# Kernel tuning notes

Measured on AMD Instinct MI355X. Metric: run time of the kernel, lower is better.

The kernel has to match this reference:

```python
import jax, jax.numpy as jnp
import numpy as np

B, S, HID, NH, HD, E, K = 8, 1024, 1024, 16, 64, 8, 2
IDIM = 2 * HD  # expert internal dim
EPS = 1e-5


def layer_norm(x, g, b):
    m = jnp.mean(x, axis=-1, keepdims=True)
    v = jnp.mean(jnp.square(x - m), axis=-1, keepdims=True)
    return (x - m) * jax.lax.rsqrt(v + EPS) * g + b


def setup_inputs() -> dict:
    key = jax.random.key(0)
    ks = jax.random.split(key, 12)
    n = jax.random.normal
    return {
        "queries": n(ks[0], (B, S, HID), jnp.float32),
        "keys": n(ks[1], (B, S, HID), jnp.float32),
        "values": n(ks[2], (B, S, HID), jnp.float32),
        "memorys": n(ks[3], (B, NH, S, HD), jnp.float32),
        "Wq": n(ks[4], (HD, HD), jnp.float32) * 0.02,
        "Wk": n(ks[5], (HD, HD), jnp.float32) * 0.02,
        "Wv": n(ks[6], (HD, HD), jnp.float32) * 0.02,
        "forget_gate": n(ks[7], (HD,), jnp.float32),
        "gate_W": n(ks[8], (E, HD), jnp.float32) * 0.02,
        "gate_b": jnp.zeros((E,), jnp.float32),
        "ln1_g": jnp.ones((E, HD), jnp.float32),
        "ln1_b": jnp.zeros((E, HD), jnp.float32),
        "W1": n(ks[9], (E, IDIM, HD), jnp.float32) * 0.02,
        "ln2_g": jnp.ones((E, IDIM), jnp.float32),
        "ln2_b": jnp.zeros((E, IDIM), jnp.float32),
        "W2": n(ks[10], (E, HD, IDIM), jnp.float32) * 0.02,
        "b2": jnp.zeros((E, HD), jnp.float32),
    }


def reference(queries, keys, values, memorys, Wq, Wk, Wv, forget_gate,
              gate_W, gate_b, ln1_g, ln1_b, W1, ln2_g, ln2_b, W2, b2):
    bsz, seq, _ = queries.shape
    gelu = lambda x: jax.nn.gelu(x, approximate=False)

    # head split: [B,S,HID] -> [B,NH,S,HD]
    q = queries.reshape(bsz, seq, NH, HD).transpose(0, 2, 1, 3)
    k = keys.reshape(bsz, seq, NH, HD).transpose(0, 2, 1, 3)
    v = values.reshape(bsz, seq, NH, HD).transpose(0, 2, 1, 3)

    q_ = q @ Wq.T
    k_ = k @ Wk.T
    v_ = v @ Wv.T

    # gated memory cell
    cell = k_ * v_ + forget_gate * memorys
    current_memorys = (1.0 - forget_gate) * cell + forget_gate * memorys
    cell_values = q_ * current_memorys  # [B,NH,S,HD]

    # token-mixing MoE (per-token, over last dim)
    x = cell_values.reshape(-1, HD)  # [N, HD], N = B*NH*S
    logits = x @ gate_W.T + gate_b  # [N, E]
    topv, topi = jax.lax.top_k(logits, K)  # [N, K]
    # sparse combine weights [N, E] (raw gate values, as in the original)
    w = jnp.sum(jax.nn.one_hot(topi, E, dtype=x.dtype) * topv[..., None], axis=1)

    def expert_fwd(g1, b1, w1, g2, b2_, w2, bias2):
        h = gelu(layer_norm(x, g1, b1)) @ w1.T      # [N, IDIM]
        h = gelu(layer_norm(h, g2, b2_)) @ w2.T + bias2  # [N, HD]
        return h

    all_out = jax.vmap(expert_fwd)(ln1_g, ln1_b, W1, ln2_g, ln2_b, W2, b2)  # [E,N,HD]
    moe = jnp.einsum('ne,end->nd', w, all_out)  # [N, HD]

    token_mixing = moe.reshape(bsz, NH, seq, HD).transpose(0, 2, 1, 3).reshape(bsz, seq, NH * HD)
    return token_mixing, current_memorys
```

## Files before the change

### kernel.cpp

```cpp
#include <hip/hip_runtime.h>
#include <stdint.h>

typedef unsigned short u16;
typedef unsigned int   u32;
typedef unsigned long long u64;
typedef __attribute__((ext_vector_type(8))) short short8;
typedef __attribute__((ext_vector_type(4))) short s16x4;
typedef __attribute__((ext_vector_type(4))) float f32x4;

#define B_    8
#define S_    1024
#define HID_  1024
#define NH_   16
#define HD_   64
#define E_    8
#define IDIM_ 128
#define NTOK  (B_*NH_*S_)

#define CSTRIDE 16

__device__ __forceinline__ float bf2f(u16 u){ return __uint_as_float(((u32)u) << 16); }
__device__ __forceinline__ u16 f2bf(float f){
    u32 u = __float_as_uint(f);
    u32 r = u + 0x7fffu + ((u >> 16) & 1u);
    return (u16)(r >> 16);
}
__device__ __forceinline__ short8 frag8(const float* __restrict__ p){
    float4 a = *(const float4*)p;
    float4 b = *(const float4*)(p + 4);
    short8 r;
    r[0]=(short)f2bf(a.x); r[1]=(short)f2bf(a.y); r[2]=(short)f2bf(a.z); r[3]=(short)f2bf(a.w);
    r[4]=(short)f2bf(b.x); r[5]=(short)f2bf(b.y); r[6]=(short)f2bf(b.z); r[7]=(short)f2bf(b.w);
    return r;
}
__device__ __forceinline__ float gelu_exact(float x){
    return 0.5f * x * (1.0f + erff(x * 0.70710678118654752f));
}
__device__ __forceinline__ float gelu_f(float x){
    float z = 1.5957691216057308f * (x + 0.044715f * x * x * x);
    float e = __expf(z);
    float t = 1.0f - 2.0f / (e + 1.0f);
    return 0.5f * x * (1.0f + t);
}

__global__ void k_zero(u32* c){
    c[threadIdx.x] = 0;
}

__global__ __launch_bounds__(256) void k_prep(
    const float* __restrict__ W1, const float* __restrict__ W2,
    u16* __restrict__ wB1, u16* __restrict__ wB2, u32* __restrict__ counters)
{
    const int i = blockIdx.x*256 + threadIdx.x;
    if (blockIdx.x == 0) counters[threadIdx.x] = 0;
    wB1[i] = f2bf(W1[i]);
    wB2[i] = f2bf(W2[i]);
}

__global__ __launch_bounds__(256,4) void k_proj(
    const float* __restrict__ qin, const float* __restrict__ kin, const float* __restrict__ vin,
    const float* __restrict__ mem,
    const float* __restrict__ Wq, const float* __restrict__ Wk, const float* __restrict__ Wv,
    const float* __restrict__ fg,
    float* __restrict__ cur_out, float* __restrict__ out0)
{
    const int lane = threadIdx.x & 63;
    const int wid  = threadIdx.x >> 6;
    const int m    = lane & 15;
    const int kg   = lane >> 4;

    const int slab  = blockIdx.x;
    const int chunk = slab & 7, h = (slab >> 3) & 15, b = slab >> 7;
    const int tw    = chunk*128 + wid*32;

    const float* kbase = kin + ((size_t)b*S_)*HID_ + h*64;
    const float* vbase = vin + ((size_t)b*S_)*HID_ + h*64;
    const float* qbase = qin + ((size_t)b*S_)*HID_ + h*64;

    f32x4 accK[2][4], accV[2][4];
    const f32x4 z = {0.f,0.f,0.f,0.f};
    #pragma unroll
    for (int i=0;i<2;i++){ accK[i][0]=z;accK[i][1]=z;accK[i][2]=z;accK[i][3]=z;
                           accV[i][0]=z;accV[i][1]=z;accV[i][2]=z;accV[i][3]=z; }

    #pragma unroll
    for (int kk=0; kk<2; kk++){
        const int k0 = kk*32 + kg*8;
        short8 aF[2], bF[4];
        #pragma unroll
        for (int mt=0; mt<2; mt++) aF[mt] = frag8(kbase + (size_t)(tw + mt*16 + m)*HID_ + k0);
        #pragma unroll
        for (int ct=0; ct<4; ct++) bF[ct] = frag8(Wk + (ct*16 + m)*64 + k0);
        #pragma unroll
        for (int mt=0; mt<2; mt++)
            #pragma unroll
            for (int ct=0; ct<4; ct++)
                accK[mt][ct] = __builtin_amdgcn_mfma_f32_16x16x32_bf16(aF[mt], bF[ct], accK[mt][ct], 0,0,0);
    }
    #pragma unroll
    for (int kk=0; kk<2; kk++){
        const int k0 = kk*32 + kg*8;
        short8 aF[2], bF[4];
        #pragma unroll
        for (int mt=0; mt<2; mt++) aF[mt] = frag8(vbase + (size_t)(tw + mt*16 + m)*HID_ + k0);
        #pragma unroll
        for (int ct=0; ct<4; ct++) bF[ct] = frag8(Wv + (ct*16 + m)*64 + k0);
        #pragma unroll
        for (int mt=0; mt<2; mt++)
            #pragma unroll
            for (int ct=0; ct<4; ct++)
                accV[mt][ct] = __builtin_amdgcn_mfma_f32_16x16x32_bf16(aF[mt], bF[ct], accV[mt][ct], 0,0,0);
    }

    const size_t nb = ((size_t)(b*NH_ + h)) << 10;
    float fgv[4];
    #pragma unroll
    for (int ct=0; ct<4; ct++) fgv[ct] = fg[ct*16 + m];

    #pragma unroll
    for (int mt=0; mt<2; mt++){
        #pragma unroll
        for (int r=0; r<4; r++){
            const int tok = tw + mt*16 + kg*4 + r;
            const size_t rowo = (nb + (size_t)tok)*64;
            #pragma unroll
            for (int ct=0; ct<4; ct++){
                const int d = ct*16 + m;
                const float kd = accK[mt][ct][r];
                const float vd = accV[mt][ct][r];
                const float f  = fgv[ct];
                const float mv = mem[rowo + d];
                const float cell = kd*vd + f*mv;
                const float cur  = (1.0f - f)*cell + f*mv;
                accK[mt][ct][r] = cur;
                cur_out[rowo + d] = cur;
            }
        }
    }

    f32x4 accQ[2][4];
    #pragma unroll
    for (int i=0;i<2;i++){ accQ[i][0]=z;accQ[i][1]=z;accQ[i][2]=z;accQ[i][3]=z; }

    #pragma unroll
    for (int kk=0; kk<2; kk++){
        const int k0 = kk*32 + kg*8;
        short8 aF[2], bF[4];
        #pragma unroll
        for (int mt=0; mt<2; mt++) aF[mt] = frag8(qbase + (size_t)(tw + mt*16 + m)*HID_ + k0);
        #pragma unroll
        for (int ct=0; ct<4; ct++) bF[ct] = frag8(Wq + (ct*16 + m)*64 + k0);
        #pragma unroll
        for (int mt=0; mt<2; mt++)
            #pragma unroll
            for (int ct=0; ct<4; ct++)
                accQ[mt][ct] = __builtin_amdgcn_mfma_f32_16x16x32_bf16(aF[mt], bF[ct], accQ[mt][ct], 0,0,0);
    }

    #pragma unroll
    for (int mt=0; mt<2; mt++){
        #pragma unroll
        for (int r=0; r<4; r++){
            const int tok = tw + mt*16 + kg*4 + r;
            const size_t po = ((size_t)(b*S_ + tok)*NH_ + h)*64;
            #pragma unroll
            for (int ct=0; ct<4; ct++){
                const int d = ct*16 + m;
                out0[po + d] = accQ[mt][ct][r] * accK[mt][ct][r];
            }
        }
    }
}

__global__ __launch_bounds__(256,2) void k_gate(
    float* __restrict__ x_io, const float* __restrict__ gW, const float* __restrict__ gB,
    const float* __restrict__ l1g, const float* __restrict__ l1b,
    uint4* __restrict__ topiv, u32* __restrict__ counts, int writeXg)
{
    __shared__ float sGW[512], sGB[8], sG1[512], sB1g[512];
    __shared__ u32 sWc[4][8];
    const int tid = threadIdx.x;
    for (int i = tid; i < 512; i += 256){ sGW[i] = gW[i]; sG1[i] = l1g[i]; sB1g[i] = l1b[i]; }
    if (tid < 8) sGB[tid] = gB[tid];
    __syncthreads();

    const int n = blockIdx.x*256 + tid;
    const int s = n & (S_-1), h = (n >> 10) & (NH_-1), b = n >> 14;
    const int pos = (b*S_ + s)*NH_ + h;
    float* rowp = x_io + ((size_t)pos << 6);

    float xr[64];
    float lg[8];
    #pragma unroll
    for (int e = 0; e < 8; e++) lg[e] = sGB[e];
    float s0 = 0.f, s1 = 0.f;

    #pragma unroll
    for (int dc = 0; dc < 16; dc++){
        float4 x4 = ((const float4*)rowp)[dc];
        xr[dc*4+0]=x4.x; xr[dc*4+1]=x4.y; xr[dc*4+2]=x4.z; xr[dc*4+3]=x4.w;
        s0 += x4.x + x4.y + x4.z + x4.w;
        s1 += x4.x*x4.x + x4.y*x4.y + x4.z*x4.z + x4.w*x4.w;
        float xv[4] = {x4.x, x4.y, x4.z, x4.w};
        #pragma unroll
        for (int i = 0; i < 4; i++){
            const int d = dc*4 + i;
            #pragma unroll
            for (int e = 0; e < 8; e++) lg[e] += sGW[e*64 + d] * xv[i];
        }
    }

    int i1 = 0; float v1 = lg[0];
    #pragma unroll
    for (int e = 1; e < 8; e++){ if (lg[e] > v1){ v1 = lg[e]; i1 = e; } }
    int i2 = -1; float v2 = -3.0e38f;
    #pragma unroll
    for (int e = 0; e < 8; e++){ if (e != i1 && lg[e] > v2){ v2 = lg[e]; i2 = e; } }

    topiv[n] = make_uint4((u32)i1, (u32)i2, __float_as_uint(v1), __float_as_uint(v2));

    if (writeXg){
        const float mu = s0 * (1.0f/64.0f);
        const float rs = rsqrtf(s1 * (1.0f/64.0f) - mu*mu + 1e-5f);
        u16* xgrow = (u16*)x_io + ((size_t)pos << 7);
        #pragma unroll
        for (int half = 0; half < 2; half++){
            const int ee = half ? i2 : i1;
            const float* g1 = &sG1[ee*64];
            const float* b1 = &sB1g[ee*64];
            uint4* dst = (uint4*)(xgrow + half*64);
            #pragma unroll
            for (int dc = 0; dc < 8; dc++){
                float vv[8];
                #pragma unroll
                for (int j = 0; j < 8; j++){
                    const int d = dc*8 + j;
                    vv[j] = gelu_f((xr[d] - mu)*rs*g1[d] + b1[d]);
                }
                uint4 o;
                o.x = (u32)f2bf(vv[0]) | ((u32)f2bf(vv[1]) << 16);
                o.y = (u32)f2bf(vv[2]) | ((u32)f2bf(vv[3]) << 16);
                o.z = (u32)f2bf(vv[4]) | ((u32)f2bf(vv[5]) << 16);
                o.w = (u32)f2bf(vv[6]) | ((u32)f2bf(vv[7]) << 16);
                dst[dc] = o;
            }
        }
    }

    const int lane = tid & 63;
    const int w    = tid >> 6;
    #pragma unroll
    for (int e = 0; e < 8; e++){
        u64 m1 = __ballot(i1 == e);
        u64 m2 = __ballot(i2 == e);
        if (lane == 0) sWc[w][e] = (u32)(__popcll(m1) + __popcll(m2));
    }
    __syncthreads();
    if (tid < 8){
        u32 t = sWc[0][tid] + sWc[1][tid] + sWc[2][tid] + sWc[3][tid];
        if (t) atomicAdd(&counts[tid*CSTRIDE], t);
    }
}

__global__ __launch_bounds__(256,2) void k_scatter(
    const uint4* __restrict__ topiv, const u32* __restrict__ counts, u32* __restrict__ cursors,
    u32* __restrict__ bucket, int2* __restrict__ slots)
{
    __shared__ u32 sC1[4][8], sC2[4][8];
    __shared__ u32 sB1[4][8], sB2w[4][8];

    const int tid = threadIdx.x;
    const int n = blockIdx.x*256 + tid;
    uint4 t = topiv[n];
    const int i1 = (int)t.x, i2 = (int)t.y;

    int off[8]; int acc = 0;
    #pragma unroll
    for (int e = 0; e < 8; e++){ off[e] = acc; acc += (int)counts[e*CSTRIDE]; }

    const int s = n & (S_-1), h = (n >> 10) & (NH_-1), b = n >> 14;
    const u32 pos32 = (u32)((b*S_ + s)*NH_ + h);

    const int lane = tid & 63;
    const int w    = tid >> 6;
    const u64 low = (1ull << lane) - 1ull;

    u64 myM1 = 0, myM2 = 0;
    #pragma unroll
    for (int e = 0; e < 8; e++){
        u64 m1 = __ballot(i1 == e);
        u64 m2 = __ballot(i2 == e);
        if (i1 == e) myM1 = m1;
        if (i2 == e) myM2 = m2;
        if (lane == 0){ sC1[w][e] = (u32)__popcll(m1); sC2[w][e] = (u32)__popcll(m2); }
    }
    __syncthreads();

    if (tid < 8){
        const int e = tid;
        u32 tot = 0;
        #pragma unroll
        for (int ww = 0; ww < 4; ww++) tot += sC1[ww][e] + sC2[ww][e];
        u32 base = tot ? atomicAdd(&cursors[e*CSTRIDE], tot) : 0;
        u32 run = base;
        #pragma unroll
        for (int ww = 0; ww < 4; ww++){
            sB1[ww][e] = run; run += sC1[ww][e];
            sB2w[ww][e] = run; run += sC2[ww][e];
        }
    }
    __syncthreads();

    const int slot1 = off[i1] + (int)sB1[w][i1] + (int)__popcll(myM1 & low);
    const int slot2 = off[i2] + (int)sB2w[w][i2] + (int)__popcll(myM2 & low);

    bucket[slot1] = (pos32 << 1);
    bucket[slot2] = (pos32 << 1) | 1u;
    slots[n] = make_int2(slot1, slot2);
}

__global__ __launch_bounds__(256,4) void k_expert_mfma(
    const float* __restrict__ x_src, const u32* __restrict__ bucket, const u32* __restrict__ counts,
    const u16* __restrict__ wB1, const u16* __restrict__ wB2,
    const float* __restrict__ l2g, const float* __restrict__ l2b,
    const float* __restrict__ b2,  u16* __restrict__ aout)
{
    const int e = blockIdx.x >> 10;
    const int c = blockIdx.x & 1023;
    const int cnt = (int)counts[e*CSTRIDE];
    const int aBase = c * 128;
    if (aBase >= cnt) return;

    int off = 0;
    #pragma unroll
    for (int ee = 0; ee < 8; ee++){ if (ee < e) off += (int)counts[ee*CSTRIDE]; }

    __shared__ __align__(16) u16 sH[4][32*128];
    __shared__ float sL2g[128], sL2b[128], sB2[64];

    const int tid = threadIdx.x;
    if (tid < 128){ sL2g[tid] = l2g[e*128+tid]; sL2b[tid] = l2b[e*128+tid]; }
    else if (tid < 192){ sB2[tid-128] = b2[e*64 + tid-128]; }
    __syncthreads();

    const int lane = tid & 63;
    const int w    = tid >> 6;
    const int m    = lane & 15;
    const int kg   = lane >> 4;
    const int tb   = aBase + w*32;
    char* sHw = (char*)(&sH[w][0]);

    const u16* xg = (const u16*)x_src;
    short8 aF[2][2];
    #pragma unroll
    for (int t = 0; t < 2; t++){
        int a = tb + t*16 + m; if (a > cnt-1) a = cnt-1;
        const u32 bv = bucket[off + a];
        const u16* rp = xg + (((size_t)(bv >> 1)) << 7) + (bv & 1u)*64;
        aF[t][0] = *(const short8*)(rp + kg*8);
        aF[t][1] = *(const short8*)(rp + 32 + kg*8);
    }

    const f32x4 z = {0.f,0.f,0.f,0.f};
    f32x4 acc1[2][8];
    #pragma unroll
    for (int t = 0; t < 2; t++)
        #pragma unroll
        for (int ct = 0; ct < 8; ct++) acc1[t][ct] = z;

    const u16* wB1e = wB1 + e*8192;
    #pragma unroll
    for (int kk = 0; kk < 2; kk++){
        const int k0 = kk*32 + kg*8;
        short8 bF[8];
        #pragma unroll
        for (int ct = 0; ct < 8; ct++)
            bF[ct] = *(const short8*)(wB1e + (ct*16 + m)*64 + k0);
        #pragma unroll
        for (int t = 0; t < 2; t++)
            #pragma unroll
            for (int ct = 0; ct < 8; ct++)
                acc1[t][ct] = __builtin_amdgcn_mfma_f32_16x16x32_bf16(aF[t][kk], bF[ct], acc1[t][ct], 0,0,0);
    }

    #pragma unroll
    for (int t = 0; t < 2; t++){
        #pragma unroll
        for (int r = 0; r < 4; r++){
            float p0 = 0.f, p1 = 0.f;
            #pragma unroll
            for (int ct = 0; ct < 8; ct++){ float v = acc1[t][ct][r]; p0 += v; p1 += v*v; }
            #pragma unroll
            for (int msk = 1; msk < 16; msk <<= 1){
                p0 += __shfl_xor(p0, msk);
                p1 += __shfl_xor(p1, msk);
            }
            const float mu = p0 * (1.0f/128.0f);
            const float rs = rsqrtf(p1 * (1.0f/128.0f) - mu*mu + 1e-5f);
            const int row = t*16 + kg*4 + r;
            #pragma unroll
            for (int ct = 0; ct < 8; ct++){
                const int col = ct*16 + m;
                *(u16*)(sHw + (((row<<8) + (col<<1)) ^ ((row&7)<<4)))
                    = f2bf(gelu_f((acc1[t][ct][r] - mu)*rs*sL2g[col] + sL2b[col]));
            }
        }
    }

    f32x4 acc2[2][4];
    #pragma unroll
    for (int t = 0; t < 2; t++)
        #pragma unroll
        for (int ct = 0; ct < 4; ct++) acc2[t][ct] = z;

    const u16* wB2e = wB2 + e*8192;
    #pragma unroll
    for (int kk = 0; kk < 4; kk++){
        const int k0 = kk*32 + kg*8;
        short8 aF2[2], bF2[4];
        #pragma unroll
        for (int t = 0; t < 2; t++){
            const int row = t*16 + m;
            aF2[t] = *(const short8*)(sHw + (((row<<8) + (k0<<1)) ^ ((row&7)<<4)));
        }
        #pragma unroll
        for (int ct = 0; ct < 4; ct++)
            bF2[ct] = *(const short8*)(wB2e + (ct*16 + m)*128 + k0);
        #pragma unroll
        for (int t = 0; t < 2; t++)
            #pragma unroll
            for (int ct = 0; ct < 4; ct++)
                acc2[t][ct] = __builtin_amdgcn_mfma_f32_16x16x32_bf16(aF2[t], bF2[ct], acc2[t][ct], 0,0,0);
    }

    #pragma unroll
    for (int t = 0; t < 2; t++){
        #pragma unroll
        for (int r = 0; r < 4; r++){
            const int row = t*16 + kg*4 + r;
            #pragma unroll
            for (int ct = 0; ct < 4; ct++){
                const int col = ct*16 + m;
                *(u16*)(sHw + (((row<<7) + (col<<1)) ^ ((row&7)<<4)))
                    = f2bf(acc2[t][ct][r] + sB2[col]);
            }
        }
    }

    #pragma unroll
    for (int it = 0; it < 4; it++){
        const int idx = it*64 + lane;
        const int row = idx >> 3, qq = idx & 7;
        if (tb + row < cnt){
            uint4 v = *(const uint4*)(sHw + (((row<<7) + (qq<<4)) ^ ((row&7)<<4)));
            *(uint4*)(aout + ((size_t)(off + tb + row) << 6) + qq*8) = v;
        }
    }
}

__global__ __launch_bounds__(256,2) void k_expert(
    const float* __restrict__ x_src, const u32* __restrict__ bucket, const u32* __restrict__ counts,
    const float* __restrict__ W1,  const float* __restrict__ W2,
    const float* __restrict__ l1g, const float* __restrict__ l1b,
    const float* __restrict__ l2g, const float* __restrict__ l2b,
    const float* __restrict__ b2,  u16* __restrict__ aout)
{
    const int e = blockIdx.x >> 9;
    const int c = blockIdx.x & 511;
    const int cnt = (int)counts[e*CSTRIDE];
    const int aBase = c * 256;
    if (aBase >= cnt) return;

    int off = 0;
    for (int ee = 0; ee < 8; ee++){ if (ee < e) off += (int)counts[ee*CSTRIDE]; }

    __shared__ float sW1[8192];
    __shared__ float sW2T[128*68];
    __shared__ float sL1g[64], sL1b[64], sL2g[128], sL2b[128], sB2[64];
    const int tid = threadIdx.x;
    for (int i = tid; i < 8192; i += 256){
        sW1[i] = W1[e*8192 + i];
        int d = i >> 7, j = i & 127;
        sW2T[j*68 + d] = W2[e*8192 + i];
    }
    if (tid < 64){ sL1g[tid] = l1g[e*64+tid]; sL1b[tid] = l1b[e*64+tid]; sB2[tid] = b2[e*64+tid]; }
    if (tid < 128){ sL2g[tid] = l2g[e*128+tid]; sL2b[tid] = l2b[e*128+tid]; }
    __syncthreads();

    const int a = aBase + tid;
    if (a >= cnt) return;
    const u32 pos32 = bucket[off + a] >> 1;

    float g[64];
    #pragma unroll
    for (int i = 0; i < 16; i++){
        float4 t = ((const float4*)(x_src + (size_t)pos32*64))[i];
        g[i*4+0]=t.x; g[i*4+1]=t.y; g[i*4+2]=t.z; g[i*4+3]=t.w;
    }

    float s0 = 0.f, s1 = 0.f;
    #pragma unroll
    for (int d = 0; d < 64; d++){ s0 += g[d]; s1 += g[d]*g[d]; }
    float m  = s0 * (1.0f/64.0f);
    float va = s1 * (1.0f/64.0f) - m*m;
    float rs = rsqrtf(va + 1e-5f);
    #pragma unroll
    for (int d = 0; d < 64; d++) g[d] = gelu_exact((g[d]-m)*rs*sL1g[d] + sL1b[d]);

    u32 hpk[64];
    float hs = 0.f, hs2 = 0.f;
    for (int jp = 0; jp < 64; jp++){
        float h0, h1;
        {
            float a0=0.f,a1=0.f,a2=0.f,a3=0.f;
            const float4* w4 = (const float4*)&sW1[(2*jp)*64];
            #pragma unroll
            for (int i = 0; i < 16; i++){
                float4 ww = w4[i];
                a0 += ww.x*g[i*4+0]; a1 += ww.y*g[i*4+1]; a2 += ww.z*g[i*4+2]; a3 += ww.w*g[i*4+3];
            }
            h0 = (a0+a1)+(a2+a3);
        }
        {
            float a0=0.f,a1=0.f,a2=0.f,a3=0.f;
            const float4* w4 = (const float4*)&sW1[(2*jp+1)*64];
            #pragma unroll
            for (int i = 0; i < 16; i++){
                float4 ww = w4[i];
                a0 += ww.x*g[i*4+0]; a1 += ww.y*g[i*4+1]; a2 += ww.z*g[i*4+2]; a3 += ww.w*g[i*4+3];
            }
            h1 = (a0+a1)+(a2+a3);
        }
        hs += h0 + h1; hs2 += h0*h0 + h1*h1;
        hpk[jp] = (u32)f2bf(h0) | ((u32)f2bf(h1) << 16);
    }
    float m2  = hs  * (1.0f/128.0f);
    float va2 = hs2 * (1.0f/128.0f) - m2*m2;
    float rs2 = rsqrtf(va2 + 1e-5f);

    float acc[64];
    #pragma unroll
    for (int d = 0; d < 64; d++) acc[d] = sB2[d];
    for (int j = 0; j < 128; j++){
        float hj = bf2f((u16)((j & 1) ? (hpk[j>>1] >> 16) : (hpk[j>>1] & 0xffffu)));
        float gh = gelu_exact((hj - m2)*rs2*sL2g[j] + sL2b[j]);
        const float4* w2t = (const float4*)&sW2T[j*68];
        #pragma unroll
        for (int d4 = 0; d4 < 16; d4++){
            float4 w = w2t[d4];
            acc[d4*4+0] += gh * w.x;
            acc[d4*4+1] += gh * w.y;
            acc[d4*4+2] += gh * w.z;
            acc[d4*4+3] += gh * w.w;
        }
    }

    u16* op = aout + (size_t)(off + a) * 64;
    #pragma unroll
    for (int dc = 0; dc < 8; dc++){
        uint4 o;
        o.x = (u32)f2bf(acc[dc*8+0]) | ((u32)f2bf(acc[dc*8+1]) << 16);
        o.y = (u32)f2bf(acc[dc*8+2]) | ((u32)f2bf(acc[dc*8+3]) << 16);
        o.z = (u32)f2bf(acc[dc*8+4]) | ((u32)f2bf(acc[dc*8+5]) << 16);
        o.w = (u32)f2bf(acc[dc*8+6]) | ((u32)f2bf(acc[dc*8+7]) << 16);
        ((uint4*)op)[dc] = o;
    }
}

__global__ __launch_bounds__(256,4) void k_combine(
    const u16* __restrict__ aout, const uint4* __restrict__ topiv,
    const int2* __restrict__ slots, float* __restrict__ out0)
{
    const int tid = threadIdx.x;
    const int p   = blockIdx.x*16 + (tid >> 4);
    const int cq  = tid & 15;

    const int h  = p & (NH_-1);
    const int bs = p >> 4;
    const int b  = bs >> 10, s = bs & (S_-1);
    const int n  = ((b*NH_ + h) << 10) + s;

    uint4 t = topiv[n];
    float w1 = __uint_as_float(t.z), w2 = __uint_as_float(t.w);
    int2 sl = slots[n];

    uint2 ua = *(const uint2*)(aout + (size_t)sl.x*64 + cq*4);
    uint2 ub = *(const uint2*)(aout + (size_t)sl.y*64 + cq*4);

    float4 o;
    o.x = w1*bf2f((u16)(ua.x & 0xffffu)) + w2*bf2f((u16)(ub.x & 0xffffu));
    o.y = w1*bf2f((u16)(ua.x >> 16))     + w2*bf2f((u16)(ub.x >> 16));
    o.z = w1*bf2f((u16)(ua.y & 0xffffu)) + w2*bf2f((u16)(ub.y & 0xffffu));
    o.w = w1*bf2f((u16)(ua.y >> 16))     + w2*bf2f((u16)(ub.y >> 16));
    *(float4*)(out0 + (size_t)p*64 + cq*4) = o;
}

extern "C" void kernel_launch(void* const* d_in, const int* in_sizes, int n_in,
                              void* d_out, int out_size, void* d_ws, size_t ws_size,
                              hipStream_t stream)
{
    const float* qin = (const float*)d_in[0];
    const float* kin = (const float*)d_in[1];
    const float* vin = (const float*)d_in[2];
    const float* mem = (const float*)d_in[3];
    const float* Wq  = (const float*)d_in[4];
    const float* Wk  = (const float*)d_in[5];
    const float* Wv  = (const float*)d_in[6];
    const float* fg  = (const float*)d_in[7];
    const float* gW  = (const float*)d_in[8];
    const float* gB  = (const float*)d_in[9];
    const float* l1g = (const float*)d_in[10];
    const float* l1b = (const float*)d_in[11];
    const float* W1  = (const float*)d_in[12];
    const float* l2g = (const float*)d_in[13];
    const float* l2b = (const float*)d_in[14];
    const float* W2  = (const float*)d_in[15];
    const float* b2  = (const float*)d_in[16];

    float* out0 = (float*)d_out;
    float* out1 = out0 + (size_t)NTOK * 64;

    char* ws = (char*)d_ws;
    u16*   aout   = (u16*)(ws);
    uint4* topiv  = (uint4*)(ws + (size_t)33554432);
    int2*  slots  = (int2*)(ws + (size_t)35651584);
    u32*   bucket = (u32*)(ws + (size_t)36700160);
    u32*   counts = (u32*)(ws + (size_t)37748736);
    u32*   cursors = (u32*)(ws + (size_t)37749248);
    u16*   wB1    = (u16*)(ws + (size_t)37749760);
    u16*   wB2    = (u16*)(ws + (size_t)37880832);
    const size_t WS_NEED = 38011904;

    (void)in_sizes; (void)n_in; (void)out_size;

    const bool use_mfma = (ws_size >= WS_NEED);

    if (use_mfma)
        k_prep <<<256, 256, 0, stream>>>(W1, W2, wB1, wB2, counts);
    else
        k_zero <<<1, 256, 0, stream>>>(counts);
    k_proj   <<<1024, 256, 0, stream>>>(qin, kin, vin, mem, Wq, Wk, Wv, fg, out1, out0);
    k_gate   <<<NTOK/256, 256, 0, stream>>>(out0, gW, gB, l1g, l1b, topiv, counts,
                                            use_mfma ? 1 : 0);
    k_scatter<<<NTOK/256, 256, 0, stream>>>(topiv, counts, cursors, bucket, slots);
    if (use_mfma)
        k_expert_mfma<<<E_*1024, 256, 0, stream>>>(out0, bucket, counts, wB1, wB2,
                                                   l2g, l2b, b2, aout);
    else
        k_expert <<<E_*512, 256, 0, stream>>>(out0, bucket, counts, W1, W2,
                                              l1g, l1b, l2g, l2b, b2, aout);
    k_combine<<<NTOK/16, 256, 0, stream>>>(aout, topiv, slots, out0);
}
```

Baseline: 348.4 us.

## Stage gate-kernel rows through padded LDS for coalesced loads and stores

The gate kernel now maps each block to consecutive rows in memory order instead of consecutive token indices. Whole row tiles are loaded into a padded shared-memory buffer with coalesced float4 accesses, and the bf16 GELU output is staged in the same buffer before being written back coalesced. Previously each thread read and wrote its own 256-byte row with strided per-thread accesses. The cost is about 66KB of LDS per block, which may limit occupancy below the declared 2 blocks per CU, and an extra barrier. The topiv index is remapped accordingly.

```diff
diff --git a/kernel.cpp b/kernel.cpp
--- a/kernel.cpp
+++ b/kernel.cpp
@@ -18,6 +18,7 @@
 #define NTOK  (B_*NH_*S_)
 
 #define CSTRIDE 16
+#define XROW 65
 
 __device__ __forceinline__ float bf2f(u16 u){ return __uint_as_float(((u32)u) << 16); }
 __device__ __forceinline__ u16 f2bf(float f){
@@ -177,37 +178,54 @@
     const float* __restrict__ l1g, const float* __restrict__ l1b,
     uint4* __restrict__ topiv, u32* __restrict__ counts, int writeXg)
 {
-    __shared__ float sGW[512], sGB[8], sG1[512], sB1g[512];
+    __shared__ float sX[256*XROW];
+    __shared__ float sGW[512], sGB[8];
+    __shared__ float sG1[8*XROW], sB1g[8*XROW];
     __shared__ u32 sWc[4][8];
+
     const int tid = threadIdx.x;
-    for (int i = tid; i < 512; i += 256){ sGW[i] = gW[i]; sG1[i] = l1g[i]; sB1g[i] = l1b[i]; }
+    for (int i = tid; i < 512; i += 256){
+        sGW[i] = gW[i];
+        const int e = i >> 6, d = i & 63;
+        sG1[e*XROW+d] = l1g[i]; sB1g[e*XROW+d] = l1b[i];
+    }
     if (tid < 8) sGB[tid] = gB[tid];
+
+    const int rowBase = blockIdx.x * 256;
+    const float* gsrc = x_io + ((size_t)rowBase << 6);
+    #pragma unroll
+    for (int j = 0; j < 16; j++){
+        const int idx = j*256 + tid;
+        const int row = idx >> 4, dc = idx & 15;
+        float4 v = ((const float4*)gsrc)[idx];
+        float* p = &sX[row*XROW + dc*4];
+        p[0]=v.x; p[1]=v.y; p[2]=v.z; p[3]=v.w;
+    }
     __syncthreads();
 
-    const int n = blockIdx.x*256 + tid;
-    const int s = n & (S_-1), h = (n >> 10) & (NH_-1), b = n >> 14;
-    const int pos = (b*S_ + s)*NH_ + h;
-    float* rowp = x_io + ((size_t)pos << 6);
-
-    float xr[64];
+    const int pos = rowBase + tid;
+    const int h  = pos & (NH_-1);
+    const int bs = pos >> 4;
+    const int s  = bs & (S_-1), b = bs >> 10;
+    const int n  = ((b*NH_ + h) << 10) + s;
+
+    float rx[64];
+    {
+        const float* xr = &sX[tid*XROW];
+        #pragma unroll
+        for (int d = 0; d < 64; d++) rx[d] = xr[d];
+    }
+
     float lg[8];
     #pragma unroll
     for (int e = 0; e < 8; e++) lg[e] = sGB[e];
     float s0 = 0.f, s1 = 0.f;
-
-    #pragma unroll
-    for (int dc = 0; dc < 16; dc++){
-        float4 x4 = ((const float4*)rowp)[dc];
-        xr[dc*4+0]=x4.x; xr[dc*4+1]=x4.y; xr[dc*4+2]=x4.z; xr[dc*4+3]=x4.w;
-        s0 += x4.x + x4.y + x4.z + x4.w;
-        s1 += x4.x*x4.x + x4.y*x4.y + x4.z*x4.z + x4.w*x4.w;
-        float xv[4] = {x4.x, x4.y, x4.z, x4.w};
-        #pragma unroll
-        for (int i = 0; i < 4; i++){
-            const int d = dc*4 + i;
-            #pragma unroll
-            for (int e = 0; e < 8; e++) lg[e] += sGW[e*64 + d] * xv[i];
-        }
+    #pragma unroll
+    for (int d = 0; d < 64; d++){
+        const float xv = rx[d];
+        s0 += xv; s1 += xv*xv;
+        #pragma unroll
+        for (int e = 0; e < 8; e++) lg[e] += sGW[e*64 + d] * xv;
     }
 
     int i1 = 0; float v1 = lg[0];
@@ -218,47 +236,53 @@
     for (int e = 0; e < 8; e++){ if (e != i1 && lg[e] > v2){ v2 = lg[e]; i2 = e; } }
 
     topiv[n] = make_uint4((u32)i1, (u32)i2, __float_as_uint(v1), __float_as_uint(v2));
+
+    {
+        const int lane = tid & 63;
+        const int w    = tid >> 6;
+        #pragma unroll
+        for (int e = 0; e < 8; e++){
+            u64 m1 = __ballot(i1 == e);
+            u64 m2 = __ballot(i2 == e);
+            if (lane == 0) sWc[w][e] = (u32)(__popcll(m1) + __popcll(m2));
+        }
+    }
 
     if (writeXg){
         const float mu = s0 * (1.0f/64.0f);
         const float rs = rsqrtf(s1 * (1.0f/64.0f) - mu*mu + 1e-5f);
-        u16* xgrow = (u16*)x_io + ((size_t)pos << 7);
+        u32* xw = (u32*)&sX[tid*XROW];
         #pragma unroll
         for (int half = 0; half < 2; half++){
             const int ee = half ? i2 : i1;
-            const float* g1 = &sG1[ee*64];
-            const float* b1 = &sB1g[ee*64];
-            uint4* dst = (uint4*)(xgrow + half*64);
-            #pragma unroll
-            for (int dc = 0; dc < 8; dc++){
-                float vv[8];
-                #pragma unroll
-                for (int j = 0; j < 8; j++){
-                    const int d = dc*8 + j;
-                    vv[j] = gelu_f((xr[d] - mu)*rs*g1[d] + b1[d]);
-                }
-                uint4 o;
-                o.x = (u32)f2bf(vv[0]) | ((u32)f2bf(vv[1]) << 16);
-                o.y = (u32)f2bf(vv[2]) | ((u32)f2bf(vv[3]) << 16);
-                o.z = (u32)f2bf(vv[4]) | ((u32)f2bf(vv[5]) << 16);
-                o.w = (u32)f2bf(vv[6]) | ((u32)f2bf(vv[7]) << 16);
-                dst[dc] = o;
-            }
-        }
-    }
-
-    const int lane = tid & 63;
-    const int w    = tid >> 6;
-    #pragma unroll
-    for (int e = 0; e < 8; e++){
-        u64 m1 = __ballot(i1 == e);
-        u64 m2 = __ballot(i2 == e);
-        if (lane == 0) sWc[w][e] = (u32)(__popcll(m1) + __popcll(m2));
+            const float* g1 = &sG1[ee*XROW];
+            const float* b1 = &sB1g[ee*XROW];
+            #pragma unroll
+            for (int dp = 0; dp < 32; dp++){
+                const float v0 = gelu_f((rx[2*dp+0] - mu)*rs*g1[2*dp+0] + b1[2*dp+0]);
+                const float vb = gelu_f((rx[2*dp+1] - mu)*rs*g1[2*dp+1] + b1[2*dp+1]);
+                xw[half*32 + dp] = (u32)f2bf(v0) | ((u32)f2bf(vb) << 16);
+            }
+        }
     }
     __syncthreads();
+
     if (tid < 8){
         u32 t = sWc[0][tid] + sWc[1][tid] + sWc[2][tid] + sWc[3][tid];
         if (t) atomicAdd(&counts[tid*CSTRIDE], t);
+    }
+
+    if (writeXg){
+        u16* gdst = (u16*)x_io + ((size_t)rowBase << 7);
+        #pragma unroll
+        for (int j = 0; j < 16; j++){
+            const int idx = j*256 + tid;
+            const int row = idx >> 4, dc = idx & 15;
+            const u32* p = (const u32*)&sX[row*XROW] + dc*4;
+            uint4 v;
+            v.x = p[0]; v.y = p[1]; v.z = p[2]; v.w = p[3];
+            ((uint4*)gdst)[idx] = v;
+        }
     }
 }
 
```

New measurement: 335.7 us. 1.04x faster.
